# Optimization experiments

Hardware: AMD Instinct MI355X
Metric: run time of the kernel (lower is better)

The kernel has to match this reference:

```python
import jax, jax.numpy as jnp
import numpy as np

N_NODES = 100000
N_EDGES = 1600000
D_IN = 128
D_HID = 128
D_OUT = 10
N_GRAPHS = 512


def _sage_conv(x, src, dst, W_l, b_l, W_r, num_nodes):
    # PyG SAGEConv (mean aggr): out = lin_l(mean_{j in N(i)} x_j) + lin_r(x_i)
    msg = x[src]                                            # [E, D] gather
    s = jax.ops.segment_sum(msg, dst, num_segments=num_nodes)
    cnt = jax.ops.segment_sum(jnp.ones((src.shape[0], 1), x.dtype), dst,
                              num_segments=num_nodes)
    mean = s / jnp.maximum(cnt, 1.0)                        # 0 where no neighbors
    return mean @ W_l.T + b_l + x @ W_r.T


def setup_inputs() -> dict:
    key = jax.random.key(0)
    ks = jax.random.split(key, 10)
    glorot = lambda k, o, i: jax.random.normal(k, (o, i), jnp.float32) * (1.0 / np.sqrt(i))
    return {
        "x": jax.random.normal(ks[0], (N_NODES, D_IN), jnp.float32),
        "edge_index": jax.random.randint(ks[1], (2, N_EDGES), 0, N_NODES, jnp.int64),
        "batch": jnp.sort(jax.random.randint(ks[2], (N_NODES,), 0, N_GRAPHS, jnp.int64)),
        "W1_l": glorot(ks[3], D_HID, D_IN),
        "b1": jnp.zeros((D_HID,), jnp.float32),
        "W1_r": glorot(ks[4], D_HID, D_IN),
        "W2_l": glorot(ks[5], D_HID, D_HID),
        "b2": jnp.zeros((D_HID,), jnp.float32),
        "W2_r": glorot(ks[6], D_HID, D_HID),
        "Wf": glorot(ks[7], D_OUT, D_HID),
        "bf": jnp.zeros((D_OUT,), jnp.float32),
    }


def reference(x, edge_index, batch, W1_l, b1, W1_r, W2_l, b2, W2_r, Wf, bf):
    src, dst = edge_index[0], edge_index[1]
    n = x.shape[0]
    h = jax.nn.relu(_sage_conv(x, src, dst, W1_l, b1, W1_r, n))
    h = jax.nn.relu(_sage_conv(h, src, dst, W2_l, b2, W2_r, n))
    # global_mean_pool over graph ids
    gsum = jax.ops.segment_sum(h, batch, num_segments=N_GRAPHS)
    gcnt = jax.ops.segment_sum(jnp.ones((n, 1), h.dtype), batch, num_segments=N_GRAPHS)
    g = gsum / jnp.maximum(gcnt, 1.0)
    logits = g @ Wf.T + bf
    return jax.nn.log_softmax(logits, axis=-1)
```

## Files before the change

kernel.cpp:

```cpp
#include <hip/hip_runtime.h>
#include <hip/hip_bf16.h>

#define N_NODES 100000
#define N_EDGES 1600000
#define N_GRAPHS 512
#define NB 256
#define NPB 391
#define CHUNK 6250
#define STAGE 7680
#define GGROUPS 1563
#define GGRID 512

typedef __attribute__((ext_vector_type(8))) short short8;
typedef __attribute__((ext_vector_type(4))) float f32x4;
typedef __attribute__((ext_vector_type(2))) float f32x2;

__device__ __forceinline__ float b2f(ushort u) {
    union { unsigned int i; float f; } c; c.i = ((unsigned int)u) << 16; return c.f;
}
__device__ __forceinline__ float blo(unsigned int u) {
    union { unsigned int i; float f; } c; c.i = u << 16; return c.f;
}
__device__ __forceinline__ float bhi(unsigned int u) {
    union { unsigned int i; float f; } c; c.i = u & 0xffff0000u; return c.f;
}
__device__ __forceinline__ ushort f2b(float f) {
    union { float f; unsigned int i; } c; c.f = f;
    unsigned int r = (c.i + 0x7fffu + ((c.i >> 16) & 1u)) >> 16;
    return (ushort)r;
}
__device__ __forceinline__ unsigned int fbits(float f) {
    union { float f; unsigned int i; } c; c.f = f; return c.i;
}
__device__ __forceinline__ int idx_at(const void* p, long i, int f) {
    return f ? (int)((const long long*)p)[i] : ((const int*)p)[i];
}
__device__ __forceinline__ short8 dec8(const uchar* p) {
    uint2 q = *(const uint2*)p;
    f32x2 d0 = __builtin_amdgcn_cvt_pk_f32_fp8((int)q.x, false);
    f32x2 d1 = __builtin_amdgcn_cvt_pk_f32_fp8((int)q.x, true);
    f32x2 d2 = __builtin_amdgcn_cvt_pk_f32_fp8((int)q.y, false);
    f32x2 d3 = __builtin_amdgcn_cvt_pk_f32_fp8((int)q.y, true);
    union { short8 s; unsigned int u[4]; } r;
    r.u[0] = __builtin_amdgcn_perm(fbits(d0.y), fbits(d0.x), 0x07060302u);
    r.u[1] = __builtin_amdgcn_perm(fbits(d1.y), fbits(d1.x), 0x07060302u);
    r.u[2] = __builtin_amdgcn_perm(fbits(d2.y), fbits(d2.x), 0x07060302u);
    r.u[3] = __builtin_amdgcn_perm(fbits(d3.y), fbits(d3.x), 0x07060302u);
    return r.s;
}

__global__ __launch_bounds__(256) void k_detect(const unsigned int* __restrict__ xw,
                                                const unsigned int* __restrict__ ew,
                                                const int* __restrict__ bw,
                                                int* __restrict__ flags) {
    __shared__ int cf, ce, cb;
    int t = threadIdx.x;
    if (t == 0) { cf = 0; ce = 0; cb = 0; }
    __syncthreads();
    unsigned int w = xw[t];
    unsigned int e = (w >> 7) & 0xffu;
    if (e >= 110u && e <= 130u) atomicAdd(&cf, 1);
    if (t < 128) {
        if (ew[2 * t + 1] != 0u) atomicAdd(&ce, 1);
        if (bw[99001 + 2 * t] != 0) atomicAdd(&cb, 1);
    }
    __syncthreads();
    if (t == 0) {
        flags[0] = (cf >= 128) ? 1 : 0;
        flags[1] = (ce == 0) ? 1 : 0;
        flags[2] = (cb == 0) ? 1 : 0;
    }
}

__global__ __launch_bounds__(256) void k_prep(const void* __restrict__ ei,
                                              const void* __restrict__ x,
                                              unsigned int* __restrict__ xf8,
                                              const void* W1l, const void* W1r,
                                              const void* W2l, const void* W2r,
                                              const void* b1,  const void* b2,
                                              ushort* __restrict__ wbf,
                                              int* __restrict__ blkcnt,
                                              float* __restrict__ gsum,
                                              const int* __restrict__ flags) {
    int b = blockIdx.x, t = threadIdx.x;
    if (b < NB) {
        __shared__ int h[NB];
        int f = flags[1];
        for (int j = t; j < NB; j += 256) h[j] = 0;
        __syncthreads();
        int lo = b * CHUNK, hi = lo + CHUNK;
        for (int e = lo + t; e < hi; e += 256) {
            int d = idx_at(ei, (long)N_EDGES + e, f);
            atomicAdd(&h[d / NPB], 1);
        }
        __syncthreads();
        if (t < NB) blkcnt[b * NB + t] = h[t];
    } else if (b < NB + 2048) {
        bool f32src = (flags[0] == 0);
        int vb = b - NB;
        const long nG = (long)N_NODES * 128 / 4;
        for (long g = (long)vb * 256 + t; g < nG; g += 2048L * 256) {
            float v0, v1, v2, v3;
            if (f32src) {
                float4 vv = ((const float4*)x)[g];
                v0 = vv.x; v1 = vv.y; v2 = vv.z; v3 = vv.w;
            } else {
                uint2 q = ((const uint2*)x)[g];
                v0 = blo(q.x); v1 = bhi(q.x); v2 = blo(q.y); v3 = bhi(q.y);
            }
            int r = __builtin_amdgcn_cvt_pk_fp8_f32(v0, v1, 0, false);
            r = __builtin_amdgcn_cvt_pk_fp8_f32(v2, v3, r, true);
            xf8[g] = (unsigned int)r;
        }
    } else if (b < NB + 2048 + 257) {
        int idx = (b - NB - 2048) * 256 + t;
        if (idx >= 65792) return;
        const void* src; int off;
        if      (idx < 16384) { src = W1l; off = idx; }
        else if (idx < 32768) { src = W1r; off = idx - 16384; }
        else if (idx < 49152) { src = W2l; off = idx - 32768; }
        else if (idx < 65536) { src = W2r; off = idx - 49152; }
        else if (idx < 65664) { src = b1;  off = idx - 65536; }
        else                  { src = b2;  off = idx - 65664; }
        wbf[idx] = (flags[0] != 0) ? ((const ushort*)src)[off]
                                   : f2b(((const float*)src)[off]);
    } else {
        int idx = (b - NB - 2048 - 257) * 256 + t;
        gsum[idx] = 0.f;
    }
}

__global__ __launch_bounds__(NB) void k_bscan(const int* __restrict__ blkcnt,
                                              int* __restrict__ bucketBase,
                                              int* __restrict__ blkbase) {
    __shared__ int s[NB];
    int t = threadIdx.x;
    int tot = 0;
    for (int blk = 0; blk < NB; ++blk) tot += blkcnt[blk * NB + t];
    s[t] = tot; __syncthreads();
    for (int off = 1; off < NB; off <<= 1) {
        int a = (t >= off) ? s[t - off] : 0;
        __syncthreads();
        s[t] += a;
        __syncthreads();
    }
    int excl = s[t] - tot;
    bucketBase[t] = excl;
    if (t == NB - 1) bucketBase[NB] = s[NB - 1];
    int run = excl;
    for (int blk = 0; blk < NB; ++blk) {
        blkbase[blk * NB + t] = run;
        run += blkcnt[blk * NB + t];
    }
}

__global__ __launch_bounds__(256) void k_bin(const void* __restrict__ ei,
                                             const int* __restrict__ blkbase,
                                             int* __restrict__ binned,
                                             const int* __restrict__ flags) {
    __shared__ int bb[NB];
    __shared__ int rank[NB];
    int t = threadIdx.x, blk = blockIdx.x;
    int f = flags[1];
    for (int j = t; j < NB; j += 256) { bb[j] = blkbase[blk * NB + j]; rank[j] = 0; }
    __syncthreads();
    int lo = blk * CHUNK, hi = lo + CHUNK;
    for (int e = lo + t; e < hi; e += 256) {
        int s = idx_at(ei, e, f);
        int d = idx_at(ei, (long)N_EDGES + e, f);
        int b = d / NPB;
        int loc = d - b * NPB;
        int r = atomicAdd(&rank[b], 1);
        binned[bb[b] + r] = s | (loc << 20);
    }
}

__global__ __launch_bounds__(256) void k_csr(const int* __restrict__ binned,
                                             const int* __restrict__ bucketBase,
                                             int* __restrict__ rowptr,
                                             int* __restrict__ csr) {
    __shared__ int cnt[400];
    __shared__ int sc[400];
    __shared__ int sh[256];
    __shared__ int stage[STAGE];
    int t = threadIdx.x, b = blockIdx.x;
    int nodeLo = b * NPB;
    int nC = N_NODES - nodeLo; if (nC > NPB) nC = NPB;
    int eBase = bucketBase[b], eEnd = bucketBase[b + 1];

    for (int j = t; j < 400; j += 256) cnt[j] = 0;
    __syncthreads();
    for (int i = eBase + t; i < eEnd; i += 256)
        atomicAdd(&cnt[binned[i] >> 20], 1);
    __syncthreads();
    int base = t * 2;
    int v0 = (base < 400) ? cnt[base] : 0;
    int v1 = (base + 1 < 400) ? cnt[base + 1] : 0;
    int ssum = v0 + v1;
    sh[t] = ssum; __syncthreads();
    for (int off = 1; off < 256; off <<= 1) {
        int a = (t >= off) ? sh[t - off] : 0;
        __syncthreads();
        sh[t] += a;
        __syncthreads();
    }
    int pre = sh[t] - ssum;
    if (base < 400) sc[base] = pre;
    if (base + 1 < 400) sc[base + 1] = pre + v0;
    __syncthreads();
    for (int j = t; j < nC; j += 256) rowptr[nodeLo + j] = eBase + sc[j];
    if (b == NB - 1) {
        if (t == 0) rowptr[N_NODES] = eEnd;
        if (t < 64) csr[N_EDGES + t] = 0;
    }
    for (int j = t; j < 400; j += 256) cnt[j] = 0;
    __syncthreads();
    for (int i = eBase + t; i < eEnd; i += 256) {
        int p = binned[i];
        int loc = p >> 20;
        int pos = sc[loc] + atomicAdd(&cnt[loc], 1);
        int srcn = p & 0xFFFFF;
        if (pos < STAGE) stage[pos] = srcn;
        else csr[eBase + pos] = srcn;
    }
    __syncthreads();
    int eCnt = eEnd - eBase; if (eCnt > STAGE) eCnt = STAGE;
    for (int j = t; j < eCnt; j += 256) csr[eBase + j] = stage[j];
}

__global__ __launch_bounds__(256) void k_agg(const uint4* __restrict__ x8,
                                             const int* __restrict__ rowptr,
                                             const int* __restrict__ csr,
                                             uint4* __restrict__ mout) {
    int wv = blockIdx.x * 4 + (threadIdx.x >> 6);
    int lane = threadIdx.x & 63;
    int li = lane & 7;
    int node = wv * 8 + (lane >> 3);
    int beg = rowptr[node];
    int end = rowptr[node + 1];
    int deg = end - beg;
    f32x2 a2[8] = {};
    int full = deg & ~7;
    int j = 0;
    for (; j < full; j += 8) {
        int vidx = csr[beg + j + li];
        uint4 p[8];
#pragma unroll
        for (int i = 0; i < 8; ++i) {
            int idx = __shfl(vidx, i | (lane & 56));
            p[i] = x8[(long)idx * 8 + li];
        }
#pragma unroll
        for (int i = 0; i < 8; ++i) {
            a2[0] += __builtin_amdgcn_cvt_pk_f32_fp8((int)p[i].x, false);
            a2[1] += __builtin_amdgcn_cvt_pk_f32_fp8((int)p[i].x, true);
            a2[2] += __builtin_amdgcn_cvt_pk_f32_fp8((int)p[i].y, false);
            a2[3] += __builtin_amdgcn_cvt_pk_f32_fp8((int)p[i].y, true);
            a2[4] += __builtin_amdgcn_cvt_pk_f32_fp8((int)p[i].z, false);
            a2[5] += __builtin_amdgcn_cvt_pk_f32_fp8((int)p[i].z, true);
            a2[6] += __builtin_amdgcn_cvt_pk_f32_fp8((int)p[i].w, false);
            a2[7] += __builtin_amdgcn_cvt_pk_f32_fp8((int)p[i].w, true);
        }
    }
    if (j < deg) {
        int pos = beg + j + li;
        if (pos > end - 1) pos = end - 1;
        int vidx = csr[pos];
#pragma unroll
        for (int i = 0; i < 8; ++i) {
            int idx = __shfl(vidx, i | (lane & 56));
            uint4 p = x8[(long)idx * 8 + li];
            bool ok = (j + i < deg);
            unsigned int q0 = ok ? p.x : 0u;
            unsigned int q1 = ok ? p.y : 0u;
            unsigned int q2 = ok ? p.z : 0u;
            unsigned int q3 = ok ? p.w : 0u;
            a2[0] += __builtin_amdgcn_cvt_pk_f32_fp8((int)q0, false);
            a2[1] += __builtin_amdgcn_cvt_pk_f32_fp8((int)q0, true);
            a2[2] += __builtin_amdgcn_cvt_pk_f32_fp8((int)q1, false);
            a2[3] += __builtin_amdgcn_cvt_pk_f32_fp8((int)q1, true);
            a2[4] += __builtin_amdgcn_cvt_pk_f32_fp8((int)q2, false);
            a2[5] += __builtin_amdgcn_cvt_pk_f32_fp8((int)q2, true);
            a2[6] += __builtin_amdgcn_cvt_pk_f32_fp8((int)q3, false);
            a2[7] += __builtin_amdgcn_cvt_pk_f32_fp8((int)q3, true);
        }
    }
    float s = (deg > 0) ? 1.f / (float)deg : 0.f;
    uint4 o;
    int r;
    r = __builtin_amdgcn_cvt_pk_fp8_f32(a2[0].x * s, a2[0].y * s, 0, false);
    r = __builtin_amdgcn_cvt_pk_fp8_f32(a2[1].x * s, a2[1].y * s, r, true);  o.x = (unsigned int)r;
    r = __builtin_amdgcn_cvt_pk_fp8_f32(a2[2].x * s, a2[2].y * s, 0, false);
    r = __builtin_amdgcn_cvt_pk_fp8_f32(a2[3].x * s, a2[3].y * s, r, true);  o.y = (unsigned int)r;
    r = __builtin_amdgcn_cvt_pk_fp8_f32(a2[4].x * s, a2[4].y * s, 0, false);
    r = __builtin_amdgcn_cvt_pk_fp8_f32(a2[5].x * s, a2[5].y * s, r, true);  o.z = (unsigned int)r;
    r = __builtin_amdgcn_cvt_pk_fp8_f32(a2[6].x * s, a2[6].y * s, 0, false);
    r = __builtin_amdgcn_cvt_pk_fp8_f32(a2[7].x * s, a2[7].y * s, r, true);  o.w = (unsigned int)r;
    mout[(long)node * 8 + li] = o;
}

__global__ __launch_bounds__(256) void k_gemm(const uchar* __restrict__ A0f8,
                                              const uchar* __restrict__ A1f8,
                                              const ushort* __restrict__ Wl,
                                              const ushort* __restrict__ Wr,
                                              const ushort* __restrict__ bias,
                                              uchar* __restrict__ out8,
                                              float* __restrict__ gsum,
                                              const void* __restrict__ batch,
                                              const int* __restrict__ flags,
                                              int layer1) {
    __shared__ short Ws[4096 * 8];
    int t = threadIdx.x;
#pragma unroll
    for (int i = 0; i < 16; ++i) {
        int f = i * 256 + t;
        int lane = f & 63, kk = (f >> 6) & 7, tile = f >> 9;
        int o = tile * 16 + (lane & 15);
        int k0 = kk * 32 + ((lane >> 4) * 8);
        const ushort* wsrc = (k0 < 128) ? (Wl + o * 128 + k0)
                                        : (Wr + o * 128 + (k0 - 128));
        *(short8*)&Ws[f * 8] = *(const short8*)wsrc;
    }
    __syncthreads();

    int wid = t >> 6, lane = t & 63;
    int kq = (lane >> 4) * 8;
    int bflag = layer1 ? 0 : flags[2];

    for (int g = blockIdx.x; g < GGROUPS; g += GGRID) {
        long nbase = (long)g * 64 + (long)wid * 16;
        int arow = (int)nbase + (lane & 15);
        if (arow >= N_NODES) arow = N_NODES - 1;

        short8 afrag[8];
#pragma unroll
        for (int kk = 0; kk < 8; ++kk) {
            int k0 = kk * 32 + kq;
            afrag[kk] = (k0 < 128)
                ? dec8(A0f8 + (long)arow * 128 + k0)
                : dec8(A1f8 + (long)arow * 128 + (k0 - 128));
        }

        int bg[4]; int guni = 0; bool uniform = false;
        if (!layer1) {
            int bmin = 0x7fffffff, bmax = -0x7fffffff;
#pragma unroll
            for (int r = 0; r < 4; ++r) {
                long node = nbase + (lane >> 4) * 4 + r;
                if (node < N_NODES) {
                    int bb = idx_at(batch, node, bflag);
                    bg[r] = bb;
                    bmin = min(bmin, bb); bmax = max(bmax, bb);
                } else { bg[r] = 0; bmax = 0x7fffffff; }
            }
            bmin = min(bmin, __shfl_xor(bmin, 16));
            bmin = min(bmin, __shfl_xor(bmin, 32));
            bmax = max(bmax, __shfl_xor(bmax, 16));
            bmax = max(bmax, __shfl_xor(bmax, 32));
            uniform = (bmin == bmax);
            guni = bmin;
        }

#pragma unroll
        for (int tile = 0; tile < 8; ++tile) {
            f32x4 acc = {0.f, 0.f, 0.f, 0.f};
#pragma unroll
            for (int kk = 0; kk < 8; ++kk) {
                short8 bfrag = *(short8*)&Ws[((tile * 8 + kk) * 64 + lane) * 8];
                acc = __builtin_amdgcn_mfma_f32_16x16x32_bf16(afrag[kk], bfrag, acc, 0, 0, 0);
            }
            int o = tile * 16 + (lane & 15);
            float bo = b2f(bias[o]);
            if (layer1) {
#pragma unroll
                for (int r = 0; r < 4; ++r) {
                    long node = nbase + (lane >> 4) * 4 + r;
                    if (node < N_NODES) {
                        float v = acc[r] + bo;
                        v = v > 0.f ? v : 0.f;
                        int pp = __builtin_amdgcn_cvt_pk_fp8_f32(v, v, 0, false);
                        out8[node * 128 + o] = (uchar)pp;
                    }
                }
            } else if (uniform) {
                float s = 0.f;
#pragma unroll
                for (int r = 0; r < 4; ++r) {
                    float v = acc[r] + bo;
                    s += (v > 0.f ? v : 0.f);
                }
                s += __shfl_xor(s, 16);
                s += __shfl_xor(s, 32);
                if ((lane >> 4) == 0) atomicAdd(&gsum[guni * 128 + o], s);
            } else {
#pragma unroll
                for (int r = 0; r < 4; ++r) {
                    long node = nbase + (lane >> 4) * 4 + r;
                    if (node < N_NODES) {
                        float v = acc[r] + bo;
                        v = v > 0.f ? v : 0.f;
                        atomicAdd(&gsum[bg[r] * 128 + o], v);
                    }
                }
            }
        }
    }
}

__global__ __launch_bounds__(128) void k_cls(const float* __restrict__ gsum,
                                             const void* __restrict__ batch,
                                             const void* __restrict__ Wf,
                                             const void* __restrict__ bfv,
                                             void* __restrict__ outp,
                                             const int* __restrict__ flags) {
    int g = blockIdx.x, t = threadIdx.x;
    bool f32 = (flags[0] == 0);
    int b64 = flags[2];
    __shared__ int rng[2];
    __shared__ float gv[128];
    __shared__ float lg[10];
    if (t < 2) {
        int v = g + t, lo = 0, hi = N_NODES;
        while (lo < hi) {
            int mid = (lo + hi) >> 1;
            if (idx_at(batch, mid, b64) < v) lo = mid + 1; else hi = mid;
        }
        rng[t] = lo;
    }
    __syncthreads();
    int cnt = rng[1] - rng[0];
    float c = (cnt > 0) ? (float)cnt : 1.f;
    gv[t] = gsum[g * 128 + t] / c;
    __syncthreads();
    if (t < 10) {
        float s = f32 ? ((const float*)bfv)[t] : b2f(((const ushort*)bfv)[t]);
        for (int k = 0; k < 128; ++k) {
            float wv = f32 ? ((const float*)Wf)[t * 128 + k] : b2f(((const ushort*)Wf)[t * 128 + k]);
            s += gv[k] * wv;
        }
        lg[t] = s;
    }
    __syncthreads();
    if (t == 0) {
        float mx = lg[0];
        for (int i = 1; i < 10; ++i) mx = fmaxf(mx, lg[i]);
        float se = 0.f;
        for (int i = 0; i < 10; ++i) se += expf(lg[i] - mx);
        float lse = mx + logf(se);
        for (int i = 0; i < 10; ++i) {
            float v = lg[i] - lse;
            if (f32) ((float*)outp)[g * 10 + i] = v;
            else     ((ushort*)outp)[g * 10 + i] = f2b(v);
        }
    }
}

extern "C" void kernel_launch(void* const* d_in, const int* in_sizes, int n_in,
                              void* d_out, int out_size, void* d_ws, size_t ws_size,
                              hipStream_t stream) {
    const void* x     = d_in[0];
    const void* ei    = d_in[1];
    const void* batch = d_in[2];
    const void* W1l = d_in[3];
    const void* b1  = d_in[4];
    const void* W1r = d_in[5];
    const void* W2l = d_in[6];
    const void* b2  = d_in[7];
    const void* W2r = d_in[8];
    const void* Wf  = d_in[9];
    const void* bf_ = d_in[10];

    char* w = (char*)d_ws;
    int* flags      = (int*)(w + 0);
    int* rowptr     = (int*)(w + 640);
    ushort* wbf     = (ushort*)(w + 400768);
    int* csr        = (int*)(w + 532480);
    float* gsum     = (float*)(w + 6933248);
    uchar* mbuf     = (uchar*)(w + 32533248);
    int* bucketBase = (int*)(w + 32533248);
    int* blkcnt     = (int*)(w + 32534528);
    int* blkbase    = (int*)(w + 32796672);
    uchar* h1f8     = (uchar*)(w + 58133248);
    int* binned     = (int*)(w + 58133248);
    unsigned int* xf8 = (unsigned int*)(w + 70933248);

    dim3 blk256(256), blkNB(NB), blk128(128);

    k_detect<<<1, blk256, 0, stream>>>((const unsigned int*)x, (const unsigned int*)ei,
                                       (const int*)batch, flags);
    k_prep<<<NB + 2048 + 257 + 256, blk256, 0, stream>>>(ei, x, xf8,
                                                         W1l, W1r, W2l, W2r, b1, b2,
                                                         wbf, blkcnt, gsum, flags);
    k_bscan<<<1, blkNB, 0, stream>>>(blkcnt, bucketBase, blkbase);
    k_bin<<<NB, blk256, 0, stream>>>(ei, blkbase, binned, flags);
    k_csr<<<NB, blk256, 0, stream>>>(binned, bucketBase, rowptr, csr);

    int agrid = N_NODES / 8 / 4;

    k_agg<<<agrid, blk256, 0, stream>>>((const uint4*)xf8, rowptr, csr, (uint4*)mbuf);
    k_gemm<<<GGRID, blk256, 0, stream>>>(mbuf, (const uchar*)xf8,
                                         wbf + 0, wbf + 16384, wbf + 65536,
                                         h1f8, (float*)nullptr, nullptr, flags, 1);
    k_agg<<<agrid, blk256, 0, stream>>>((const uint4*)h1f8, rowptr, csr, (uint4*)mbuf);
    k_gemm<<<GGRID, blk256, 0, stream>>>(mbuf, h1f8,
                                         wbf + 32768, wbf + 49152, wbf + 65664,
                                         (uchar*)nullptr, gsum, batch, flags, 0);
    k_cls<<<N_GRAPHS, blk128, 0, stream>>>(gsum, batch, Wf, bf_, d_out, flags);
}
```

Before: 304.4 us.

## Stage GEMM A-tiles through swizzled LDS with register prefetch of next group

The fp8 A operand for each 64-row group is now loaded with coalesced 16-byte global reads into registers. It is written to an XOR-swizzled LDS buffer, and each wave reads its MFMA fragments from there. Previously every lane did its own strided 8-byte global loads. The next group's rows are prefetched into registers while the current group's MFMAs and atomics run, which hides global latency. The cost is extra LDS traffic, more register pressure, and two block barriers per iteration.

```diff
diff --git a/kernel.cpp b/kernel.cpp
--- a/kernel.cpp
+++ b/kernel.cpp
@@ -35,8 +35,7 @@
 __device__ __forceinline__ int idx_at(const void* p, long i, int f) {
     return f ? (int)((const long long*)p)[i] : ((const int*)p)[i];
 }
-__device__ __forceinline__ short8 dec8(const uchar* p) {
-    uint2 q = *(const uint2*)p;
+__device__ __forceinline__ short8 dec8v(uint2 q) {
     f32x2 d0 = __builtin_amdgcn_cvt_pk_f32_fp8((int)q.x, false);
     f32x2 d1 = __builtin_amdgcn_cvt_pk_f32_fp8((int)q.x, true);
     f32x2 d2 = __builtin_amdgcn_cvt_pk_f32_fp8((int)q.y, false);
@@ -310,36 +309,60 @@
                                               const int* __restrict__ flags,
                                               int layer1) {
     __shared__ short Ws[4096 * 8];
+    __shared__ uint4 Ast4[1024];
+    uchar* Ast = (uchar*)Ast4;
     int t = threadIdx.x;
+    int wid = t >> 6, lane = t & 63;
+
+    int g0 = blockIdx.x;
+    uint4 sreg[4];
+#pragma unroll
+    for (int c = 0; c < 4; ++c) {
+        int cid = c * 256 + t;
+        int r = (cid >> 3) & 63, lc8 = cid & 7;
+        long grow = (long)g0 * 64 + r; if (grow >= N_NODES) grow = N_NODES - 1;
+        const uchar* bp = (cid & 512) ? A1f8 : A0f8;
+        sreg[c] = *(const uint4*)(bp + grow * 128 + lc8 * 16);
+    }
+
 #pragma unroll
     for (int i = 0; i < 16; ++i) {
         int f = i * 256 + t;
-        int lane = f & 63, kk = (f >> 6) & 7, tile = f >> 9;
-        int o = tile * 16 + (lane & 15);
-        int k0 = kk * 32 + ((lane >> 4) * 8);
+        int ln = f & 63, kk = (f >> 6) & 7, tile = f >> 9;
+        int o = tile * 16 + (ln & 15);
+        int k0 = kk * 32 + ((ln >> 4) * 8);
         const ushort* wsrc = (k0 < 128) ? (Wl + o * 128 + k0)
                                         : (Wr + o * 128 + (k0 - 128));
         *(short8*)&Ws[f * 8] = *(const short8*)wsrc;
     }
-    __syncthreads();
-
-    int wid = t >> 6, lane = t & 63;
+#pragma unroll
+    for (int c = 0; c < 4; ++c) {
+        int cid = c * 256 + t;
+        int buf = cid >> 9, r = (cid >> 3) & 63, lc8 = cid & 7;
+        int sc = (buf * 8 + lc8) ^ (r & 15);
+        *(uint4*)&Ast[r * 256 + sc * 16] = sreg[c];
+    }
+    __syncthreads();
+
     int kq = (lane >> 4) * 8;
+    int lm = lane & 15, qh = (lane >> 5) & 1, ql8 = ((lane >> 4) & 1) * 8;
+    int rloc = wid * 16 + lm;
     int bflag = layer1 ? 0 : flags[2];
-
-    for (int g = blockIdx.x; g < GGROUPS; g += GGRID) {
+    (void)kq;
+
+    for (int g = g0; g < GGROUPS; g += GGRID) {
         long nbase = (long)g * 64 + (long)wid * 16;
-        int arow = (int)nbase + (lane & 15);
-        if (arow >= N_NODES) arow = N_NODES - 1;
-
-        short8 afrag[8];
-#pragma unroll
-        for (int kk = 0; kk < 8; ++kk) {
-            int k0 = kk * 32 + kq;
-            afrag[kk] = (k0 < 128)
-                ? dec8(A0f8 + (long)arow * 128 + k0)
-                : dec8(A1f8 + (long)arow * 128 + (k0 - 128));
-        }
+
+        uint2 raw[8];
+        {
+            int rb = rloc * 256 + ql8;
+#pragma unroll
+            for (int kk = 0; kk < 8; ++kk) {
+                int sc = ((kk * 2 + qh) ^ lm) << 4;
+                raw[kk] = *(const uint2*)&Ast[rb + sc];
+            }
+        }
+        __syncthreads();
 
         int bg[4]; int guni = 0; bool uniform = false;
         if (!layer1) {
@@ -360,6 +383,23 @@
             uniform = (bmin == bmax);
             guni = bmin;
         }
+
+        int gn = g + GGRID;
+        bool havenext = (gn < GGROUPS);
+        if (havenext) {
+#pragma unroll
+            for (int c = 0; c < 4; ++c) {
+                int cid = c * 256 + t;
+                int r = (cid >> 3) & 63, lc8 = cid & 7;
+                long grow = (long)gn * 64 + r; if (grow >= N_NODES) grow = N_NODES - 1;
+                const uchar* bp = (cid & 512) ? A1f8 : A0f8;
+                sreg[c] = *(const uint4*)(bp + grow * 128 + lc8 * 16);
+            }
+        }
+
+        short8 afrag[8];
+#pragma unroll
+        for (int kk = 0; kk < 8; ++kk) afrag[kk] = dec8v(raw[kk]);
 
 #pragma unroll
         for (int tile = 0; tile < 8; ++tile) {
@@ -404,6 +444,17 @@
                 }
             }
         }
+
+        if (havenext) {
+#pragma unroll
+            for (int c = 0; c < 4; ++c) {
+                int cid = c * 256 + t;
+                int buf = cid >> 9, r = (cid >> 3) & 63, lc8 = cid & 7;
+                int sc = (buf * 8 + lc8) ^ (r & 15);
+                *(uint4*)&Ast[r * 256 + sc * 16] = sreg[c];
+            }
+        }
+        __syncthreads();
     }
 }
 
```

New measurement: 297.7 us. -2.2%, faster.
